# Performance work log

Hardware: AMD Instinct MI355X
Metric: run time of the kernel (lower is better)

The kernel has to match this reference:

```python
import jax, jax.numpy as jnp
import numpy as np
from jax import lax

Z_DIM = 64
ZS_SIZE = [[1,1],[1,1],[4,1],[4,1],[1,4],[1,1],[4,1],[1,4],[1,1],[4,1],[2,4],[2,2],[8,2],[8,4],[2,8],[2,2],[8,2],[2,8],[2,2],[8,2],[2,8],[2,2],[8,2],[4,8],[4,4],[16,4],[16,8],[4,16],[4,4],[16,4],[4,16],[4,4],[16,4],[4,16],[4,4],[16,4],[4,16],[4,4],[16,4],[4,16],[4,4],[16,4],[8,16],[8,8],[32,8],[32,16],[8,32],[8,8],[32,8],[8,32],[8,8],[32,8]]
Z_TOTAL = sum(h * k for h, k in ZS_SIZE)  # 3268
SHORTCUT = {0: 1, 3: 2, 7: 2, 13: 2}  # block idx -> stride (first block of each stage)
N_BLOCKS = 16


def setup_inputs() -> dict:
    key = jax.random.key(0)
    ks = jax.random.split(key, 7)
    return {
        "x": jax.random.normal(ks[0], (64, 3, 32, 32), jnp.float32),
        "conv1_w": jax.random.normal(ks[1], (64, 3, 3, 3), jnp.float32) * 0.1,
        "z_all": jax.random.uniform(ks[2], (Z_TOTAL, Z_DIM), jnp.float32),  # torch.rand init
        "hw1": jax.random.normal(ks[3], (Z_DIM, Z_DIM * Z_DIM), jnp.float32) * 0.05,
        "hb1": jnp.zeros((Z_DIM * Z_DIM,), jnp.float32),
        "hw2": jax.random.normal(ks[4], (Z_DIM, Z_DIM * 9), jnp.float32) * 0.05,
        "hb2": jnp.zeros((Z_DIM * 9,), jnp.float32),
        "final_w": jax.random.normal(ks[5], (10, 2048), jnp.float32) * 0.02,
        "final_b": jnp.zeros((10,), jnp.float32),
    }


def _bn(x):
    # nn.BatchNorm2d in training mode with default gamma=1, beta=0
    m = x.mean((0, 2, 3), keepdims=True)
    v = x.var((0, 2, 3), keepdims=True)
    return (x - m) * lax.rsqrt(v + 1e-5)


def _conv(x, w, s):
    return lax.conv_general_dilated(x, w, (s, s), ((1, 1), (1, 1)),
                                    dimension_numbers=('NCHW', 'OIHW', 'NCHW'))


def _gen_weights(z_all, hw1, hb1, hw2, hb2):
    # Batched hypernetwork: z[N,64] -> kernels[N,64,64,3,3] in two GEMMs
    h = (z_all @ hw1 + hb1).reshape(-1, Z_DIM, Z_DIM)            # [N, out=64, z]
    k = (jnp.einsum('noz,zf->nof', h, hw2) + hb2)                # [N, 64, 576]
    k = k.reshape(-1, Z_DIM, Z_DIM, 3, 3)                        # [N, out64, in64, 3, 3]
    weights, off = [], 0
    for hh, kk in ZS_SIZE:
        blk = k[off:off + hh * kk].reshape(hh, kk, Z_DIM, Z_DIM, 3, 3)
        # Embedding: cat over j (in-channels, dim=1) then over i (out-channels, dim=0)
        blk = blk.transpose(0, 2, 1, 3, 4, 5).reshape(hh * Z_DIM, kk * Z_DIM, 3, 3)
        weights.append(blk)
        off += hh * kk
    return weights


def reference(x, conv1_w, z_all, hw1, hb1, hw2, hb2, final_w, final_b):
    weights = _gen_weights(z_all, hw1, hb1, hw2, hb2)
    out = _bn(x)                                    # data_bn
    out = jax.nn.relu(_bn(_conv(out, conv1_w, 1)))  # stem
    j = 0
    for i in range(N_BLOCKS):
        w1, w2, w3 = weights[j], weights[j + 1], weights[j + 2]
        if i in SHORTCUT:
            ws, s = weights[j + 3], SHORTCUT[i]
            j += 4
        else:
            ws, s = None, 1
            j += 3
        o = jax.nn.relu(_bn(_conv(out, w1, 1)))
        o = jax.nn.relu(_bn(_conv(o, w2, s)))
        o = _bn(_conv(o, w3, 1))
        sc = _bn(_conv(out, ws, s)) if ws is not None else out
        out = jax.nn.relu(o + sc)
    pooled = out.mean((2, 3))                        # AdaptiveAvgPool2d(1) + squeeze
    return pooled @ final_w.T + final_b
```

## Files before the change

kernel.cpp:

```cpp
#include <hip/hip_runtime.h>
#include <hip/hip_fp16.h>

#define TPB 256

typedef _Float16 f16;
typedef __attribute__((ext_vector_type(8))) _Float16 f16x8;
typedef __attribute__((ext_vector_type(4))) float f32x4;

__global__ void k_prep_hw1(const float* __restrict__ hw1, f16* __restrict__ hw1T) {
  int idx = blockIdx.x * TPB + threadIdx.x;
  if (idx >= 4096 * 64) return;
  int z = idx & 63, n = idx >> 6;
  hw1T[idx] = (f16)hw1[z * 4096 + n];
}

__global__ void k_prep_hw2(const float* __restrict__ hw2, const float* __restrict__ hb2,
                           f16* __restrict__ hw2T, float* __restrict__ b2T,
                           float* __restrict__ stz, float* __restrict__ mvxz) {
  int idx = blockIdx.x * TPB + threadIdx.x;
  if (idx < 128) stz[idx] = 0.f;
  if (idx < 8) mvxz[idx] = 0.f;
  if (idx >= 576 * 64) return;
  int z = idx & 63, j = idx >> 6;
  int tap = j >> 6, c = j & 63;
  hw2T[(size_t)j * 64 + z] = (f16)hw2[z * 576 + c * 9 + tap];
  if (z == 0) b2T[j] = hb2[c * 9 + tap];
}

__global__ void k_prep_stemw(const float* __restrict__ w, f16* __restrict__ sw) {
  int idx = blockIdx.x * TPB + threadIdx.x;
  if (idx >= 10 * 64 * 64) return;
  int ci = idx & 63, co = (idx >> 6) & 63, tap = idx >> 12;
  float v = 0.f;
  if (tap < 9 && ci < 3) v = w[co * 27 + ci * 9 + tap];
  sw[idx] = (f16)v;
}

__global__ __launch_bounds__(256) void k_gen_h_mfma(
    const float* __restrict__ z, const f16* __restrict__ hw1T, const float* __restrict__ hb1,
    f16* __restrict__ h, int M) {
  __shared__ f16 As[256 * 64];
  __shared__ f16 Bs[64 * 64];
  const int t = threadIdx.x, lane = t & 63, wid = t >> 6;
  const int m0 = blockIdx.x * 256;
  const int n0 = blockIdx.y * 64;
  char* AsB = (char*)As;
  char* BsB = (char*)Bs;
  {
    int row = t;
    bool ok = (m0 + row) < M;
    const float* src = z + (size_t)(m0 + row) * 64;
#pragma unroll
    for (int ch = 0; ch < 8; ch++) {
      f16x8 v = {};
      if (ok) {
        f32x4 a = *(const f32x4*)(src + ch * 8);
        f32x4 b = *(const f32x4*)(src + ch * 8 + 4);
#pragma unroll
        for (int q = 0; q < 4; q++) { v[q] = (f16)a[q]; v[q + 4] = (f16)b[q]; }
      }
      *(f16x8*)(AsB + row * 128 + ((ch ^ (row & 7)) << 4)) = v;
    }
  }
  {
#pragma unroll
    for (int q = 0; q < 2; q++) {
      int id = t + q * 256;
      int row = id >> 3, ch = id & 7;
      f16x8 v = *(const f16x8*)(hw1T + ((size_t)(n0 + row)) * 64 + ch * 8);
      *(f16x8*)(BsB + row * 128 + ((ch ^ (row & 7)) << 4)) = v;
    }
  }
  __syncthreads();
  f32x4 acc[4][4];
#pragma unroll
  for (int m = 0; m < 4; m++)
#pragma unroll
    for (int n = 0; n < 4; n++) acc[m][n] = (f32x4){0.f, 0.f, 0.f, 0.f};
#pragma unroll
  for (int ks = 0; ks < 2; ks++) {
    f16x8 af[4], bf[4];
#pragma unroll
    for (int m = 0; m < 4; m++) {
      int row = wid * 64 + m * 16 + (lane & 15);
      int c = ks * 4 + (lane >> 4);
      af[m] = *(const f16x8*)(AsB + row * 128 + ((c ^ (row & 7)) << 4));
    }
#pragma unroll
    for (int n = 0; n < 4; n++) {
      int row = n * 16 + (lane & 15);
      int c = ks * 4 + (lane >> 4);
      bf[n] = *(const f16x8*)(BsB + row * 128 + ((c ^ (row & 7)) << 4));
    }
#pragma unroll
    for (int m = 0; m < 4; m++)
#pragma unroll
      for (int n = 0; n < 4; n++)
        acc[m][n] = __builtin_amdgcn_mfma_f32_16x16x32_f16(af[m], bf[n], acc[m][n], 0, 0, 0);
  }
#pragma unroll
  for (int n = 0; n < 4; n++) {
    int c = n * 16 + (lane & 15);
    float bj = hb1[n0 + c];
#pragma unroll
    for (int m = 0; m < 4; m++) {
      int rbase = m0 + wid * 64 + m * 16 + (lane >> 4) * 4;
#pragma unroll
      for (int r = 0; r < 4; r++) {
        int row = rbase + r;
        if (row < M) h[(size_t)row * 4096 + n0 + c] = (f16)(acc[m][n][r] + bj);
      }
    }
  }
}

__global__ __launch_bounds__(256) void k_gen_w(
    const f16* __restrict__ h, const f16* __restrict__ hw2T, const float* __restrict__ b2T,
    f16* __restrict__ wout, int hoff, int M, int l2kk, int Cin, int Cout,
    float* __restrict__ st, int stClr) {
  __shared__ f16 As[256 * 64];
  __shared__ f16 Bs[64 * 64];
  const int t = threadIdx.x, lane = t & 63, wid = t >> 6;
  const int m0 = blockIdx.x * 256;
  const int tap = blockIdx.y;
  char* AsB = (char*)As;
  char* BsB = (char*)Bs;
  if (blockIdx.x == 0 && blockIdx.y == 0)
    for (int i = t; i < stClr; i += 256) st[i] = 0.f;
  {
    int row = t;
    const f16* src = h + (size_t)(hoff + m0 + row) * 64;
    bool ok = (m0 + row) < M;
#pragma unroll
    for (int ch = 0; ch < 8; ch++) {
      f16x8 v = {};
      if (ok) v = *(const f16x8*)(src + ch * 8);
      *(f16x8*)(AsB + row * 128 + ((ch ^ (row & 7)) << 4)) = v;
    }
  }
  {
#pragma unroll
    for (int q = 0; q < 2; q++) {
      int id = t + q * 256;
      int row = id >> 3, ch = id & 7;
      f16x8 v = *(const f16x8*)(hw2T + ((size_t)tap * 64 + row) * 64 + ch * 8);
      *(f16x8*)(BsB + row * 128 + ((ch ^ (row & 7)) << 4)) = v;
    }
  }
  __syncthreads();
  f32x4 acc[4][4];
#pragma unroll
  for (int m = 0; m < 4; m++)
#pragma unroll
    for (int n = 0; n < 4; n++) acc[m][n] = (f32x4){0.f, 0.f, 0.f, 0.f};
#pragma unroll
  for (int ks = 0; ks < 2; ks++) {
    f16x8 af[4], bf[4];
#pragma unroll
    for (int m = 0; m < 4; m++) {
      int row = wid * 64 + m * 16 + (lane & 15);
      int c = ks * 4 + (lane >> 4);
      af[m] = *(const f16x8*)(AsB + row * 128 + ((c ^ (row & 7)) << 4));
    }
#pragma unroll
    for (int n = 0; n < 4; n++) {
      int row = n * 16 + (lane & 15);
      int c = ks * 4 + (lane >> 4);
      bf[n] = *(const f16x8*)(BsB + row * 128 + ((c ^ (row & 7)) << 4));
    }
#pragma unroll
    for (int m = 0; m < 4; m++)
#pragma unroll
      for (int n = 0; n < 4; n++)
        acc[m][n] = __builtin_amdgcn_mfma_f32_16x16x32_f16(af[m], bf[n], acc[m][n], 0, 0, 0);
  }
  const int kkm1 = (1 << l2kk) - 1;
#pragma unroll
  for (int n = 0; n < 4; n++) {
    int c = n * 16 + (lane & 15);
    float bj = b2T[tap * 64 + c];
#pragma unroll
    for (int m = 0; m < 4; m++) {
      int rbase = m0 + wid * 64 + m * 16 + (lane >> 4) * 4;
#pragma unroll
      for (int r = 0; r < 4; r++) {
        int row = rbase + r;
        if (row < M) {
          int o = row & 63, g = row >> 6;
          int i = g >> l2kk, jb = g & kkm1;
          wout[((size_t)tap * Cout + (i << 6) + o) * Cin + (jb << 6) + c] =
              (f16)(acc[m][n][r] + bj);
        }
      }
    }
  }
}

template <int FUSE>
__global__ __launch_bounds__(512) void k_conv_mfma(
    const f16* __restrict__ in, f16* __restrict__ outh, float* __restrict__ outf,
    const f16* __restrict__ wt, float* __restrict__ stats,
    int Cin, int Cout, int Hin, int l2W, int l2HW, int stride, int KS) {
  __shared__ f16 As[128 * 64];
  __shared__ f16 Bs[128 * 64];
  __shared__ float bns[256];

  const int t = threadIdx.x;
  const int lane = t & 63;
  const int wid = t >> 6;
  const int wm = wid >> 2, wn = wid & 3;

  const int gx = gridDim.x;
  const int nwg = gx * gridDim.y;
  const int flat = blockIdx.y * gx + blockIdx.x;
  const int qq = nwg >> 3, rr = nwg & 7;
  const int xcd = flat & 7, ii = flat >> 3;
  const int swz = (xcd < rr ? xcd * (qq + 1) : rr * (qq + 1) + (xcd - rr) * qq) + ii;
  const int m0 = (swz % gx) * 128, co0 = (swz / gx) * 128;

  if (FUSE && t < 256) bns[t] = 0.f;

  const int r0 = t >> 3;
  const int ch = t & 7;
  int pn[2], py[2], px[2];
#pragma unroll
  for (int q = 0; q < 2; q++) {
    int pix = m0 + r0 + q * 64;
    pn[q] = pix >> l2HW;
    int prem = pix & ((1 << l2HW) - 1);
    py[q] = prem >> l2W;
    px[q] = prem & ((1 << l2W) - 1);
  }
  char* AsB = (char*)As;
  char* BsB = (char*)Bs;
  const int aw0 = r0 * 128 + ((ch ^ (r0 & 7)) << 4);
  const int aw1 = (r0 + 64) * 128 + ((ch ^ (r0 & 7)) << 4);

  int aro[4][2], bro[2][2];
#pragma unroll
  for (int m = 0; m < 4; m++) {
    int row = wm * 64 + m * 16 + (lane & 15);
#pragma unroll
    for (int ks = 0; ks < 2; ks++) {
      int c = ks * 4 + (lane >> 4);
      aro[m][ks] = row * 128 + ((c ^ (row & 7)) << 4);
    }
  }
#pragma unroll
  for (int n = 0; n < 2; n++) {
    int row = wn * 32 + n * 16 + (lane & 15);
#pragma unroll
    for (int ks = 0; ks < 2; ks++) {
      int c = ks * 4 + (lane >> 4);
      bro[n][ks] = row * 128 + ((c ^ (row & 7)) << 4);
    }
  }

  f32x4 acc[4][2];
#pragma unroll
  for (int m = 0; m < 4; m++)
#pragma unroll
    for (int n = 0; n < 2; n++) acc[m][n] = (f32x4){0.f, 0.f, 0.f, 0.f};

  const int ck = Cin >> 6;
  const int S = 9 * ck;
  int sBeg = 0, sEnd = S;
  if (!FUSE) {
    sBeg = (int)(((long)blockIdx.z * S) / KS);
    sEnd = (int)(((long)(blockIdx.z + 1) * S) / KS);
  }
  int tap = sBeg / ck;
  int kin = (sBeg - tap * ck) << 6;
  int dy = tap / 3, dx = tap - dy * 3;

  const f16* aptr[2];
  bool aok[2];
  const f16* bptr[2];
  auto setTap = [&]() {
#pragma unroll
    for (int q = 0; q < 2; q++) {
      int iy = py[q] * stride + dy - 1;
      int ix = px[q] * stride + dx - 1;
      aok[q] = ((unsigned)iy < (unsigned)Hin) && ((unsigned)ix < (unsigned)Hin);
      aptr[q] = in + (((size_t)pn[q] * Hin + iy) * Hin + ix) * Cin + ch * 8;
      bptr[q] = wt + ((size_t)tap * Cout + co0 + r0 + q * 64) * Cin + ch * 8;
    }
  };
  setTap();

  f16x8 zz = {};
  f16x8 av[2], bv[2];
#pragma unroll
  for (int q = 0; q < 2; q++) {
    av[q] = aok[q] ? *(const f16x8*)(aptr[q] + kin) : zz;
    bv[q] = *(const f16x8*)(bptr[q] + kin);
  }

  for (int s = sBeg; s < sEnd; s++) {
    __syncthreads();
    *(f16x8*)(AsB + aw0) = av[0];
    *(f16x8*)(AsB + aw1) = av[1];
    *(f16x8*)(BsB + aw0) = bv[0];
    *(f16x8*)(BsB + aw1) = bv[1];
    __syncthreads();
    if (s + 1 < sEnd) {
      kin += 64;
      if (kin == Cin) {
        kin = 0; tap++; dx++;
        if (dx == 3) { dx = 0; dy++; }
        setTap();
      }
#pragma unroll
      for (int q = 0; q < 2; q++) {
        av[q] = aok[q] ? *(const f16x8*)(aptr[q] + kin) : zz;
        bv[q] = *(const f16x8*)(bptr[q] + kin);
      }
    }
#pragma unroll
    for (int ks = 0; ks < 2; ks++) {
      f16x8 af[4], bf[2];
#pragma unroll
      for (int m = 0; m < 4; m++) af[m] = *(const f16x8*)(AsB + aro[m][ks]);
#pragma unroll
      for (int n = 0; n < 2; n++) bf[n] = *(const f16x8*)(BsB + bro[n][ks]);
#pragma unroll
      for (int m = 0; m < 4; m++)
#pragma unroll
        for (int n = 0; n < 2; n++)
          acc[m][n] = __builtin_amdgcn_mfma_f32_16x16x32_f16(af[m], bf[n], acc[m][n], 0, 0, 0);
    }
  }

  const int colL = lane & 15;
  const int rowL = (lane >> 4) * 4;
#pragma unroll
  for (int m = 0; m < 4; m++) {
    int prow = m0 + wm * 64 + m * 16 + rowL;
#pragma unroll
    for (int n = 0; n < 2; n++) {
      int col = co0 + wn * 32 + n * 16 + colL;
      if (col < Cout) {
        if (FUSE) {
#pragma unroll
          for (int r = 0; r < 4; r++)
            outh[(size_t)(prow + r) * Cout + col] = (f16)acc[m][n][r];
        } else {
#pragma unroll
          for (int r = 0; r < 4; r++)
            atomicAdd(&outf[(size_t)(prow + r) * Cout + col], acc[m][n][r]);
        }
      }
    }
  }
  if (FUSE) {
#pragma unroll
    for (int n = 0; n < 2; n++) {
      float s1 = 0.f, s2 = 0.f;
#pragma unroll
      for (int m = 0; m < 4; m++)
#pragma unroll
        for (int r = 0; r < 4; r++) { float v = acc[m][n][r]; s1 += v; s2 += v * v; }
      s1 += __shfl_xor(s1, 16); s2 += __shfl_xor(s2, 16);
      s1 += __shfl_xor(s1, 32); s2 += __shfl_xor(s2, 32);
      if (lane < 16) {
        int c = wn * 32 + n * 16 + colL;
        atomicAdd(&bns[c], s1);
        atomicAdd(&bns[128 + c], s2);
      }
    }
    __syncthreads();
    if (t < 128 && co0 + t < Cout) {
      atomicAdd(&stats[co0 + t], bns[t]);
      atomicAdd(&stats[Cout + co0 + t], bns[128 + t]);
    }
  }
}

template <typename T>
__global__ void k_bnstats_nhwc(const T* __restrict__ t, float* __restrict__ acc,
                               int C, int npix, int pps) {
  int c = blockIdx.y * 64 + (threadIdx.x & 63);
  int pr = threadIdx.x >> 6;
  int p0 = blockIdx.x * pps;
  int pend = min(p0 + pps, npix);
  float s = 0.f, s2 = 0.f;
  for (int p = p0 + pr; p < pend; p += 4) {
    float v = (float)t[(size_t)p * C + c];
    s += v; s2 += v * v;
  }
  __shared__ float sh1[256], sh2[256];
  sh1[threadIdx.x] = s; sh2[threadIdx.x] = s2;
  __syncthreads();
  if (threadIdx.x < 64) {
    s = sh1[threadIdx.x] + sh1[threadIdx.x + 64] + sh1[threadIdx.x + 128] + sh1[threadIdx.x + 192];
    s2 = sh2[threadIdx.x] + sh2[threadIdx.x + 64] + sh2[threadIdx.x + 128] + sh2[threadIdx.x + 192];
    atomicAdd(&acc[c], s);
    atomicAdd(&acc[C + c], s2);
  }
}

template <typename T>
__global__ void k_bnapply(const T* __restrict__ src, const f16* __restrict__ res,
                          f16* __restrict__ dst, const float* __restrict__ st,
                          int C, float invn, int total8, int relu) {
  int idx = blockIdx.x * TPB + threadIdx.x;
  if (idx >= total8) return;
  size_t base = (size_t)idx * 8;
  int c0 = (int)(base & (size_t)(C - 1));
  float v[8];
  if constexpr (sizeof(T) == 2) {
    f16x8 x = *(const f16x8*)(src + base);
#pragma unroll
    for (int q = 0; q < 8; q++) v[q] = (float)x[q];
  } else {
    f32x4 x0 = *(const f32x4*)(src + base);
    f32x4 x1 = *(const f32x4*)(src + base + 4);
#pragma unroll
    for (int q = 0; q < 4; q++) { v[q] = x0[q]; v[q + 4] = x1[q]; }
  }
  f16x8 rv;
  if (res) rv = *(const f16x8*)(res + base);
  f16x8 o;
#pragma unroll
  for (int q = 0; q < 8; q++) {
    int c = c0 + q;
    float mean = st[c] * invn;
    float var = st[C + c] * invn - mean * mean;
    float f = (v[q] - mean) * rsqrtf(var + 1e-5f);
    if (res) f += (float)rv[q];
    if (relu) f = fmaxf(f, 0.f);
    o[q] = (f16)f;
  }
  *(f16x8*)(dst + base) = o;
}

__global__ void k_bnstats_x(const float* __restrict__ t, float* __restrict__ mvx) {
  int n = blockIdx.x / 3, c = blockIdx.x - 3 * n;
  const float* p = t + ((size_t)n * 3 + c) * 1024;
  float s = 0.f, s2 = 0.f;
  for (int i = threadIdx.x; i < 1024; i += TPB) { float v = p[i]; s += v; s2 += v * v; }
#pragma unroll
  for (int off = 32; off > 0; off >>= 1) { s += __shfl_down(s, off); s2 += __shfl_down(s2, off); }
  __shared__ float sh[8];
  int wid = threadIdx.x >> 6;
  if ((threadIdx.x & 63) == 0) { sh[wid * 2] = s; sh[wid * 2 + 1] = s2; }
  __syncthreads();
  if (threadIdx.x == 0) {
    for (int w = 1; w < TPB / 64; w++) { s += sh[w * 2]; s2 += sh[w * 2 + 1]; }
    atomicAdd(&mvx[c], s);
    atomicAdd(&mvx[4 + c], s2);
  }
}

__global__ void k_apply_x(const float* __restrict__ src, f16* __restrict__ dst,
                          const float* __restrict__ mvx, int total) {
  int idx = blockIdx.x * TPB + threadIdx.x;
  if (idx >= total) return;
  int r = idx & 1023;
  int cch = (idx >> 10) % 3;
  int n = idx / 3072;
  const float invn = 1.f / 65536.f;
  float mean = mvx[cch] * invn;
  float var = mvx[4 + cch] * invn - mean * mean;
  float v = (src[idx] - mean) * rsqrtf(var + 1e-5f);
  dst[((size_t)(n * 1024 + r)) * 64 + cch] = (f16)v;
}

__global__ void k_poolfc(const f16* __restrict__ in, const float* __restrict__ fw,
                         const float* __restrict__ fb, float* __restrict__ out) {
  __shared__ float pooled[2048];
  __shared__ float red[4];
  int n = blockIdx.x;
  for (int c = threadIdx.x; c < 2048; c += TPB) {
    float s = 0.f;
#pragma unroll
    for (int p = 0; p < 16; p++) s += (float)in[((size_t)n * 16 + p) * 2048 + c];
    pooled[c] = s * (1.f / 16.f);
  }
  __syncthreads();
  for (int kk = 0; kk < 10; kk++) {
    float s = 0.f;
    for (int c = threadIdx.x; c < 2048; c += TPB) s += pooled[c] * fw[kk * 2048 + c];
#pragma unroll
    for (int off = 32; off > 0; off >>= 1) s += __shfl_down(s, off);
    if ((threadIdx.x & 63) == 0) red[threadIdx.x >> 6] = s;
    __syncthreads();
    if (threadIdx.x == 0) out[n * 10 + kk] = red[0] + red[1] + red[2] + red[3] + fb[kk];
    __syncthreads();
  }
}

extern "C" void kernel_launch(void* const* d_in, const int* in_sizes, int n_in,
                              void* d_out, int out_size, void* d_ws, size_t ws_size,
                              hipStream_t stream) {
  static const int ZS_H[52] = {1,1,4,4,1,1,4,1,1,4,2,2,8,8,2,2,8,2,2,8,2,2,8,4,4,16,16,
                               4,4,16,4,4,16,4,4,16,4,4,16,4,4,16,8,8,32,32,8,8,32,8,8,32};
  static const int ZS_K[52] = {1,1,1,1,4,1,1,4,1,1,4,2,2,4,8,2,2,8,2,2,8,2,2,8,4,4,8,
                               16,4,4,16,4,4,16,4,4,16,4,4,16,4,4,16,8,8,16,32,8,8,32,8,8};
  int offz[52];
  { int a = 0; for (int t = 0; t < 52; t++) { offz[t] = a; a += ZS_H[t] * ZS_K[t]; } }

  const float* x     = (const float*)d_in[0];
  const float* c1w   = (const float*)d_in[1];
  const float* z_all = (const float*)d_in[2];
  const float* hw1   = (const float*)d_in[3];
  const float* hb1   = (const float*)d_in[4];
  const float* hw2   = (const float*)d_in[5];
  const float* hb2   = (const float*)d_in[6];
  const float* fw    = (const float*)d_in[7];
  const float* fb    = (const float*)d_in[8];
  float* out = (float*)d_out;

  char* ws = (char*)d_ws;
  size_t pos = 0;
  auto take = [&](size_t b) -> char* { char* p = ws + pos; pos += (b + 255) & ~(size_t)255; return p; };
  f16*   wbuf    = (f16*)take((size_t)512 * 64 * 576 * 2);
  f16*   hbuf    = (f16*)take((size_t)3268 * 4096 * 2);
  f16*   A       = (f16*)take((size_t)16777216 * 2);
  f16*   B       = (f16*)take((size_t)16777216 * 2);
  f16*   C_      = (f16*)take((size_t)16777216 * 2);
  float* scratch = (float*)take((size_t)16 << 20);
  f16*   xn64    = (f16*)take((size_t)64 * 1024 * 64 * 2);
  float* mv      = (float*)take(2 * 2048 * 4);
  float* mv2     = (float*)take(2 * 2048 * 4);
  float* mvx     = (float*)take(8 * 4);
  f16*   hw1T    = (f16*)take((size_t)4096 * 64 * 2);
  f16*   hw2T    = (f16*)take((size_t)576 * 64 * 2);
  float* b2T     = (float*)take(576 * 4);
  f16*   stemW   = (f16*)take((size_t)10 * 64 * 64 * 2);
  if (ws_size < pos) return;

  hipMemsetAsync(xn64, 0, (size_t)64 * 1024 * 64 * 2, stream);
  k_prep_hw1<<<(4096 * 64 + TPB - 1) / TPB, TPB, 0, stream>>>(hw1, hw1T);
  k_prep_hw2<<<(576 * 64 + TPB - 1) / TPB, TPB, 0, stream>>>(hw2, hb2, hw2T, b2T, mv, mvx);
  k_prep_stemw<<<(10 * 64 * 64 + TPB - 1) / TPB, TPB, 0, stream>>>(c1w, stemW);
  k_gen_h_mfma<<<dim3(13, 64), 256, 0, stream>>>(z_all, hw1T, hb1, hbuf, 3268);

  auto genw = [&](int jj, float* st, int Cout) {
    int nr = ZS_H[jj] * ZS_K[jj];
    int CoutW = ZS_H[jj] * 64, CinW = ZS_K[jj] * 64;
    int M = nr * 64;
    int l2kk = __builtin_ctz(ZS_K[jj]);
    k_gen_w<<<dim3((unsigned)((M + 255) / 256), 9), 256, 0, stream>>>(
        hbuf, hw2T, b2T, wbuf, offz[jj] * 64, M, l2kk, CinW, CoutW, st, 2 * Cout);
  };

  auto conv = [&](const f16* src, f16* dst, int jj, int Cin, int Cout,
                  int Hin, int Hout, int s, float* st) -> bool {
    genw(jj, st, Cout);
    int M = 64 * Hout * Hout;
    int nbx = M / 128, nby = (Cout + 127) / 128;
    int ck = Cin >> 6, S = 9 * ck;
    int natural = nbx * nby;
    int l2W = (Hout == 32) ? 5 : (Hout == 16) ? 4 : (Hout == 8) ? 3 : 2;
    int ks = 1;
    if (natural < 240) {
      ks = (240 + natural - 1) / natural;
      if (ks > S) ks = S;
      if (ks > 16) ks = 16;
    }
    if (ks == 1) {
      k_conv_mfma<1><<<dim3(nbx, nby, 1), 512, 0, stream>>>(
          src, dst, nullptr, wbuf, st, Cin, Cout, Hin, l2W, 2 * l2W, s, 1);
      return false;
    } else {
      hipMemsetAsync(scratch, 0, (size_t)M * Cout * 4, stream);
      k_conv_mfma<0><<<dim3(nbx, nby, ks), 512, 0, stream>>>(
          src, nullptr, scratch, wbuf, nullptr, Cin, Cout, Hin, l2W, 2 * l2W, s, ks);
      dim3 g((unsigned)((M + 63) / 64), (unsigned)(Cout / 64));
      k_bnstats_nhwc<float><<<g, TPB, 0, stream>>>(scratch, st, Cout, M, 64);
      return true;
    }
  };

  auto applyF = [&](bool split, const f16* rawh, const f16* res, f16* dst, float* st,
                    int C, int npix, int relu) {
    int tot8 = npix * C / 8;
    int g = (tot8 + TPB - 1) / TPB;
    if (split)
      k_bnapply<float><<<g, TPB, 0, stream>>>(scratch, res, dst, st, C, 1.f / npix, tot8, relu);
    else
      k_bnapply<f16><<<g, TPB, 0, stream>>>(rawh, res, dst, st, C, 1.f / npix, tot8, relu);
  };

  k_bnstats_x<<<192, TPB, 0, stream>>>(x, mvx);
  { int tot = 64 * 3 * 1024;
    k_apply_x<<<(tot + TPB - 1) / TPB, TPB, 0, stream>>>(x, xn64, mvx, tot); }

  k_conv_mfma<1><<<dim3(512, 1, 1), 512, 0, stream>>>(
      xn64, A, nullptr, stemW, mv, 64, 64, 32, 5, 10, 1, 1);
  applyF(false, A, nullptr, A, mv, 64, 64 * 1024, 1);

  f16* P[3] = {A, B, C_};
  int cur = 0, H = 32, j = 0, cin = 64;
  for (int i = 0; i < 16; i++) {
    bool hasSc = (i == 0 || i == 3 || i == 7 || i == 13);
    int s = (hasSc && i != 0) ? 2 : 1;
    int cmid = ZS_H[j] * 64;
    int cout = ZS_H[j + 2] * 64;
    int Hin = H, Hout = H / s;
    int f1 = (cur + 1) % 3, f2 = (cur + 2) % 3;

    bool c1 = conv(P[cur], P[f1], j, cin, cmid, Hin, Hin, 1, mv);
    applyF(c1, P[f1], nullptr, P[f1], mv, cmid, 64 * Hin * Hin, 1);

    bool c2 = conv(P[f1], P[f2], j + 1, cmid, cmid, Hin, Hout, s, mv);
    applyF(c2, P[f2], nullptr, P[f2], mv, cmid, 64 * Hout * Hout, 1);

    if (hasSc) {
      bool cs = conv(P[cur], P[f1], j + 3, cin, cout, Hin, Hout, s, mv2);
      applyF(cs, P[f1], nullptr, P[f1], mv2, cout, 64 * Hout * Hout, 0);
      bool c3 = conv(P[f2], P[cur], j + 2, cmid, cout, Hout, Hout, 1, mv);
      applyF(c3, P[cur], P[f1], P[cur], mv, cout, 64 * Hout * Hout, 1);
      j += 4;
    } else {
      bool c3 = conv(P[f2], P[f1], j + 2, cmid, cout, Hout, Hout, 1, mv);
      applyF(c3, P[f1], P[cur], P[f2], mv, cout, 64 * Hout * Hout, 1);
      cur = f2;
      j += 3;
    }
    cin = cout; H = Hout;
  }

  k_poolfc<<<64, TPB, 0, stream>>>(P[cur], fw, fb, out);
}
```

Measured before the change: 3.165 ms.

## Add templated conv kernel with smaller tiles and XCD-aware block swizzle

Adds a templated implicit-GEMM conv kernel with configurable M/N tile sizes (128x64 or 64x128) and an XCD-aware workgroup remapping. Cout=64 layers use a 128x64 tile so no compute is wasted on padded columns. Layers with too few 128x128 tiles try 64x128 tiles before falling back to split-K. This aims to cut wasted MFMA work and the atomic split-K plus extra stats pass, at the cost of less operand reuse per tile and a second kernel variant to maintain.

Measured after the change: 3.050 ms. 3.6% less time.

```diff
diff --git a/kernel.cpp b/kernel.cpp
--- a/kernel.cpp
+++ b/kernel.cpp
@@ -372,6 +372,198 @@
     if (t < 128 && co0 + t < Cout) {
       atomicAdd(&stats[co0 + t], bns[t]);
       atomicAdd(&stats[Cout + co0 + t], bns[128 + t]);
+    }
+  }
+}
+
+template <int FUSE, int MT, int NT>
+__global__ __launch_bounds__(512) void k_conv_s(
+    const f16* __restrict__ in, f16* __restrict__ outh, float* __restrict__ outf,
+    const f16* __restrict__ wt, float* __restrict__ stats,
+    int Cin, int Cout, int Hin, int l2W, int l2HW, int stride, int KS) {
+  constexpr int WN = NT / 32;
+  constexpr int NA = (MT * 8) / 512;
+  constexpr int NB = (NT * 8) / 512;
+  __shared__ f16 As[MT * 64];
+  __shared__ f16 Bs[NT * 64];
+  __shared__ float bns[2 * NT];
+
+  const int t = threadIdx.x;
+  const int lane = t & 63;
+  const int wid = t >> 6;
+  const int wm = wid / WN, wn = wid % WN;
+
+  const int gx = gridDim.x;
+  const int nwg = gx * gridDim.y;
+  const int flat = blockIdx.y * gx + blockIdx.x;
+  const int qq = nwg >> 3, rr = nwg & 7;
+  const int xcd = flat & 7, ii = flat >> 3;
+  const int swz = (xcd < rr ? xcd * (qq + 1) : rr * (qq + 1) + (xcd - rr) * qq) + ii;
+  const int m0 = (swz % gx) * MT, co0 = (swz / gx) * NT;
+
+  if (FUSE && t < 2 * NT) bns[t] = 0.f;
+
+  const int r0 = t >> 3;
+  const int ch = t & 7;
+  int pn[NA], py[NA], px[NA];
+#pragma unroll
+  for (int q = 0; q < NA; q++) {
+    int pix = m0 + r0 + q * 64;
+    pn[q] = pix >> l2HW;
+    int prem = pix & ((1 << l2HW) - 1);
+    py[q] = prem >> l2W;
+    px[q] = prem & ((1 << l2W) - 1);
+  }
+  char* AsB = (char*)As;
+  char* BsB = (char*)Bs;
+  int awo[NA], bwo[NB];
+#pragma unroll
+  for (int q = 0; q < NA; q++) {
+    int row = r0 + q * 64;
+    awo[q] = row * 128 + ((ch ^ (row & 7)) << 4);
+  }
+#pragma unroll
+  for (int q = 0; q < NB; q++) {
+    int row = r0 + q * 64;
+    bwo[q] = row * 128 + ((ch ^ (row & 7)) << 4);
+  }
+
+  int aro[2][2], bro[2][2];
+#pragma unroll
+  for (int m = 0; m < 2; m++) {
+    int row = wm * 32 + m * 16 + (lane & 15);
+#pragma unroll
+    for (int ks = 0; ks < 2; ks++) {
+      int c = ks * 4 + (lane >> 4);
+      aro[m][ks] = row * 128 + ((c ^ (row & 7)) << 4);
+    }
+  }
+#pragma unroll
+  for (int n = 0; n < 2; n++) {
+    int row = wn * 32 + n * 16 + (lane & 15);
+#pragma unroll
+    for (int ks = 0; ks < 2; ks++) {
+      int c = ks * 4 + (lane >> 4);
+      bro[n][ks] = row * 128 + ((c ^ (row & 7)) << 4);
+    }
+  }
+
+  f32x4 acc[2][2];
+#pragma unroll
+  for (int m = 0; m < 2; m++)
+#pragma unroll
+    for (int n = 0; n < 2; n++) acc[m][n] = (f32x4){0.f, 0.f, 0.f, 0.f};
+
+  const int ck = Cin >> 6;
+  const int S = 9 * ck;
+  int sBeg = 0, sEnd = S;
+  if (!FUSE) {
+    sBeg = (int)(((long)blockIdx.z * S) / KS);
+    sEnd = (int)(((long)(blockIdx.z + 1) * S) / KS);
+  }
+  int tap = sBeg / ck;
+  int kin = (sBeg - tap * ck) << 6;
+  int dy = tap / 3, dx = tap - dy * 3;
+
+  const f16* aptr[NA];
+  bool aok[NA];
+  const f16* bptr[NB];
+  auto setTap = [&]() {
+#pragma unroll
+    for (int q = 0; q < NA; q++) {
+      int iy = py[q] * stride + dy - 1;
+      int ix = px[q] * stride + dx - 1;
+      aok[q] = ((unsigned)iy < (unsigned)Hin) && ((unsigned)ix < (unsigned)Hin);
+      aptr[q] = in + (((size_t)pn[q] * Hin + iy) * Hin + ix) * Cin + ch * 8;
+    }
+#pragma unroll
+    for (int q = 0; q < NB; q++)
+      bptr[q] = wt + ((size_t)tap * Cout + co0 + r0 + q * 64) * Cin + ch * 8;
+  };
+  setTap();
+
+  f16x8 zz = {};
+  f16x8 av[NA], bv[NB];
+#pragma unroll
+  for (int q = 0; q < NA; q++) av[q] = aok[q] ? *(const f16x8*)(aptr[q] + kin) : zz;
+#pragma unroll
+  for (int q = 0; q < NB; q++) bv[q] = *(const f16x8*)(bptr[q] + kin);
+
+  for (int s = sBeg; s < sEnd; s++) {
+    __syncthreads();
+#pragma unroll
+    for (int q = 0; q < NA; q++) *(f16x8*)(AsB + awo[q]) = av[q];
+#pragma unroll
+    for (int q = 0; q < NB; q++) *(f16x8*)(BsB + bwo[q]) = bv[q];
+    __syncthreads();
+    if (s + 1 < sEnd) {
+      kin += 64;
+      if (kin == Cin) {
+        kin = 0; tap++; dx++;
+        if (dx == 3) { dx = 0; dy++; }
+        setTap();
+      }
+#pragma unroll
+      for (int q = 0; q < NA; q++) av[q] = aok[q] ? *(const f16x8*)(aptr[q] + kin) : zz;
+#pragma unroll
+      for (int q = 0; q < NB; q++) bv[q] = *(const f16x8*)(bptr[q] + kin);
+    }
+#pragma unroll
+    for (int ks = 0; ks < 2; ks++) {
+      f16x8 af[2], bf[2];
+#pragma unroll
+      for (int m = 0; m < 2; m++) af[m] = *(const f16x8*)(AsB + aro[m][ks]);
+#pragma unroll
+      for (int n = 0; n < 2; n++) bf[n] = *(const f16x8*)(BsB + bro[n][ks]);
+#pragma unroll
+      for (int m = 0; m < 2; m++)
+#pragma unroll
+        for (int n = 0; n < 2; n++)
+          acc[m][n] = __builtin_amdgcn_mfma_f32_16x16x32_f16(af[m], bf[n], acc[m][n], 0, 0, 0);
+    }
+  }
+
+  const int colL = lane & 15;
+  const int rowL = (lane >> 4) * 4;
+#pragma unroll
+  for (int m = 0; m < 2; m++) {
+    int prow = m0 + wm * 32 + m * 16 + rowL;
+#pragma unroll
+    for (int n = 0; n < 2; n++) {
+      int col = co0 + wn * 32 + n * 16 + colL;
+      if (col < Cout) {
+        if (FUSE) {
+#pragma unroll
+          for (int r = 0; r < 4; r++)
+            outh[(size_t)(prow + r) * Cout + col] = (f16)acc[m][n][r];
+        } else {
+#pragma unroll
+          for (int r = 0; r < 4; r++)
+            atomicAdd(&outf[(size_t)(prow + r) * Cout + col], acc[m][n][r]);
+        }
+      }
+    }
+  }
+  if (FUSE) {
+#pragma unroll
+    for (int n = 0; n < 2; n++) {
+      float s1 = 0.f, s2 = 0.f;
+#pragma unroll
+      for (int m = 0; m < 2; m++)
+#pragma unroll
+        for (int r = 0; r < 4; r++) { float v = acc[m][n][r]; s1 += v; s2 += v * v; }
+      s1 += __shfl_xor(s1, 16); s2 += __shfl_xor(s2, 16);
+      s1 += __shfl_xor(s1, 32); s2 += __shfl_xor(s2, 32);
+      if (lane < 16) {
+        int c = wn * 32 + n * 16 + colL;
+        atomicAdd(&bns[c], s1);
+        atomicAdd(&bns[NT + c], s2);
+      }
+    }
+    __syncthreads();
+    if (t < NT && co0 + t < Cout) {
+      atomicAdd(&stats[co0 + t], bns[t]);
+      atomicAdd(&stats[Cout + co0 + t], bns[NT + t]);
     }
   }
 }
@@ -549,28 +741,35 @@
                   int Hin, int Hout, int s, float* st) -> bool {
     genw(jj, st, Cout);
     int M = 64 * Hout * Hout;
-    int nbx = M / 128, nby = (Cout + 127) / 128;
-    int ck = Cin >> 6, S = 9 * ck;
-    int natural = nbx * nby;
+    int S = 9 * (Cin >> 6);
     int l2W = (Hout == 32) ? 5 : (Hout == 16) ? 4 : (Hout == 8) ? 3 : 2;
-    int ks = 1;
-    if (natural < 240) {
-      ks = (240 + natural - 1) / natural;
-      if (ks > S) ks = S;
-      if (ks > 16) ks = 16;
-    }
-    if (ks == 1) {
-      k_conv_mfma<1><<<dim3(nbx, nby, 1), 512, 0, stream>>>(
+    if (Cout == 64) {
+      k_conv_s<1, 128, 64><<<dim3(M / 128, 1, 1), 512, 0, stream>>>(
           src, dst, nullptr, wbuf, st, Cin, Cout, Hin, l2W, 2 * l2W, s, 1);
       return false;
-    } else {
-      hipMemsetAsync(scratch, 0, (size_t)M * Cout * 4, stream);
-      k_conv_mfma<0><<<dim3(nbx, nby, ks), 512, 0, stream>>>(
-          src, nullptr, scratch, wbuf, nullptr, Cin, Cout, Hin, l2W, 2 * l2W, s, ks);
-      dim3 g((unsigned)((M + 63) / 64), (unsigned)(Cout / 64));
-      k_bnstats_nhwc<float><<<g, TPB, 0, stream>>>(scratch, st, Cout, M, 64);
-      return true;
-    }
+    }
+    int nby = (Cout + 127) / 128;
+    int nat128 = (M / 128) * nby;
+    if (nat128 >= 240) {
+      k_conv_mfma<1><<<dim3(M / 128, nby, 1), 512, 0, stream>>>(
+          src, dst, nullptr, wbuf, st, Cin, Cout, Hin, l2W, 2 * l2W, s, 1);
+      return false;
+    }
+    int nat64 = (M / 64) * nby;
+    if (nat64 >= 240) {
+      k_conv_s<1, 64, 128><<<dim3(M / 64, nby, 1), 512, 0, stream>>>(
+          src, dst, nullptr, wbuf, st, Cin, Cout, Hin, l2W, 2 * l2W, s, 1);
+      return false;
+    }
+    int ks = (240 + nat64 - 1) / nat64;
+    if (ks > S) ks = S;
+    if (ks > 16) ks = 16;
+    hipMemsetAsync(scratch, 0, (size_t)M * Cout * 4, stream);
+    k_conv_s<0, 64, 128><<<dim3(M / 64, nby, ks), 512, 0, stream>>>(
+        src, nullptr, scratch, wbuf, nullptr, Cin, Cout, Hin, l2W, 2 * l2W, s, ks);
+    dim3 g((unsigned)((M + 63) / 64), (unsigned)(Cout / 64));
+    k_bnstats_nhwc<float><<<g, TPB, 0, stream>>>(scratch, st, Cout, M, 64);
+    return true;
   };
 
   auto applyF = [&](bool split, const f16* rawh, const f16* res, f16* dst, float* st,
@@ -587,7 +786,7 @@
   { int tot = 64 * 3 * 1024;
     k_apply_x<<<(tot + TPB - 1) / TPB, TPB, 0, stream>>>(x, xn64, mvx, tot); }
 
-  k_conv_mfma<1><<<dim3(512, 1, 1), 512, 0, stream>>>(
+  k_conv_s<1, 128, 64><<<dim3(512, 1, 1), 512, 0, stream>>>(
       xn64, A, nullptr, stemW, mv, 64, 64, 32, 5, 10, 1, 1);
   applyF(false, A, nullptr, A, mv, 64, 64 * 1024, 1);
 
```
